# Optimization experiments

Measured on AMD Instinct MI355X. Metric: run time of the kernel, lower is better.

Reference implementation:

```python
import jax, jax.numpy as jnp
from jax import lax
import numpy as np

EPS = 1e-12      # F.normalize eps
TOP_N = 250      # top negatives selected
SMOOTH = 1e-5    # soft dice smooth


def _dilate10(m):
    # == 10 iterations of 3x3x3 binary max-pool dilation. m: [B,D,H,W] float.
    for _ in range(10):
        m = lax.reduce_window(m, 0.0, lax.max, (1, 3, 3, 3), (1, 1, 1, 1), 'SAME')
    return m


def _self_loss(feature, lab):
    # feature: [B,C,D,H,W], lab: [B,D,H,W] int
    feat = jnp.moveaxis(feature, 1, -1)                       # [B,D,H,W,C]
    pos = (lab == 1)
    posf = pos.astype(feat.dtype)
    cnt = posf.sum()
    std = (feat * posf[..., None]).sum((0, 1, 2, 3)) / jnp.maximum(cnt, 1.0)
    std = jnp.where(cnt > 0, std, 0.0)                        # [C]
    std_n = std / jnp.maximum(jnp.linalg.norm(std), EPS)
    feat_n = feat / jnp.maximum(jnp.linalg.norm(feat, axis=-1, keepdims=True), EPS)
    # cosine similarity of per-voxel normalized features vs normalized mean positive
    sim = jnp.einsum('bdhwc,c->bdhw', feat_n, std_n)

    # positive term: mean over positives of (1 - sim)
    pos_loss = jnp.where(cnt > 0, ((1.0 - sim) * posf).sum() / jnp.maximum(cnt, 1.0), 0.0)

    # easily-misclassified ring: dilate(pos,10) & ~pos; mean relu(sim)
    mis = (_dilate10(posf) > 0) & (~pos)
    misf = mis.astype(sim.dtype)
    mcnt = misf.sum()
    mis_loss = jnp.where(mcnt > 0, (jax.nn.relu(sim) * misf).sum() / jnp.maximum(mcnt, 1.0), 0.0)

    # hard negatives: top-250 sims among label==0, scatter to mask, dilate, & ~pos
    neg = (lab == 0)
    neg_sims = jnp.where(neg, sim, -jnp.inf).reshape(-1)
    top_vals, top_idx = lax.top_k(neg_sims, TOP_N)
    hsm = jnp.zeros(neg_sims.shape[0], sim.dtype).at[top_idx].set(
        jnp.where(jnp.isfinite(top_vals), 1.0, 0.0)).reshape(sim.shape)
    fin = (_dilate10(hsm) > 0) & (~pos)
    finf = fin.astype(sim.dtype)
    fcnt = finf.sum()
    neg_loss = jnp.where(fcnt > 0, (jax.nn.relu(sim) * finf).sum() / jnp.maximum(fcnt, 1.0), 0.0)

    return pos_loss + mis_loss + neg_loss


def _ce_dice(net_output, target):
    lab = target[:, 0]                                        # [B,D,H,W]
    logp = jax.nn.log_softmax(net_output, axis=1)
    ce = -jnp.mean(jnp.take_along_axis(logp, target, axis=1))
    probs = jnp.exp(logp)                                     # softmax_helper_dim1
    nc = net_output.shape[1]
    onehot = jax.nn.one_hot(lab, nc, axis=1, dtype=probs.dtype)  # [B,nc,D,H,W]
    axes = (0, 2, 3, 4)                                       # batch_dice=True
    tp = (probs * onehot).sum(axes)
    fp = (probs * (1.0 - onehot)).sum(axes)
    fn = ((1.0 - probs) * onehot).sum(axes)
    dc = (2.0 * tp + SMOOTH) / (2.0 * tp + fp + fn + SMOOTH + 1e-8)
    dice = -jnp.mean(dc[1:])                                  # do_bg=False
    return ce, dice


def reference(feature, net_output, target):
    ce, dice = _ce_dice(net_output, target)
    sl = _self_loss(feature, target[:, 0])
    return 1.0 * ce + 1.0 * dice + 5.0 * sl


def setup_inputs():
    key = jax.random.key(0)
    k1, k2, k3 = jax.random.split(key, 3)
    B, C, D, H, W = 2, 32, 64, 128, 128
    NC = 2
    feature = jax.random.normal(k1, (B, C, D, H, W), jnp.float32)
    net_output = jax.random.normal(k2, (B, NC, D, H, W), jnp.float32)
    target = jax.random.randint(k3, (B, 1, D, H, W), 0, 2).astype(jnp.int32)
    return {'feature': feature, 'net_output': net_output, 'target': target}
```

## Files before the change

### kernel.cpp

```cpp
#include <hip/hip_runtime.h>
#include <stdint.h>

typedef unsigned int u32;
typedef unsigned long long u64;
typedef float f4v __attribute__((ext_vector_type(4)));
typedef int i4v __attribute__((ext_vector_type(4)));

#define BB 2
#define CC 32
#define DD 64
#define HH 128
#define WW 128
#define SS (DD*HH*WW)
#define NN (BB*SS)
#define NQ (NN/4)
#define NWORDS (NN/64)
#define EPSF 1e-12f
#define TOPN 250u

struct Ctrl {
  u32 done4, tie, pad0, pad1;
};

struct Acc {
  double ce, tp, fp, fn;
  double stdsum[CC];
  double pos_num, mis_num, fin_num;
  u64 cnt, mcnt, fcnt;
};

__device__ __forceinline__ float waveRedF(float v){
#pragma unroll
  for (int o = 32; o; o >>= 1) v += __shfl_xor(v, o);
  return v;
}
__device__ __forceinline__ u32 waveRedU(u32 v){
#pragma unroll
  for (int o = 32; o; o >>= 1) v += __shfl_xor(v, o);
  return v;
}
__device__ __forceinline__ void red_d(double* dst, float v, volatile float* sh){
  int lane = threadIdx.x & 63, wid = threadIdx.x >> 6;
  v = waveRedF(v);
  if (lane == 0) sh[wid] = v;
  __syncthreads();
  if (threadIdx.x == 0){
    float t = 0.f;
    for (int i = 0; i < (int)(blockDim.x >> 6); i++) t += sh[i];
    atomicAdd(dst, (double)t);
  }
  __syncthreads();
}
__device__ __forceinline__ void red_u(u64* dst, u32 v, volatile u32* sh){
  int lane = threadIdx.x & 63, wid = threadIdx.x >> 6;
  v = waveRedU(v);
  if (lane == 0) sh[wid] = v;
  __syncthreads();
  if (threadIdx.x == 0){
    u32 t = 0;
    for (int i = 0; i < (int)(blockDim.x >> 6); i++) t += sh[i];
    atomicAdd(dst, (u64)t);
  }
  __syncthreads();
}

__device__ __forceinline__ u32 sortkey(float f){
  u32 u = __float_as_uint(f);
  return (u & 0x80000000u) ? ~u : (u | 0x80000000u);
}

__device__ __forceinline__ void select_top(const u32* __restrict__ hist, u32 nbins,
                                           u32 k, u32* shres, u32* binOut, u32* kremOut){
  __syncthreads();
  if (threadIdx.x < 64){
    int lane = threadIdx.x;
    u32 running = 0; bool found = false;
    for (u32 chunk = 0; chunk * 64 < nbins && !found; chunk++){
      int bin = (int)nbins - 1 - (int)(chunk * 64 + (u32)lane);
      u32 val = (bin >= 0) ? hist[bin] : 0u;
      u32 p = val;
#pragma unroll
      for (int o = 1; o < 64; o <<= 1){ u32 t = __shfl_up(p, o); if (lane >= o) p += t; }
      u32 tot = __shfl(p, 63);
      u32 incl = running + p, excl = incl - val;
      bool hit = (excl < k) && (incl >= k);
      u64 mb = __ballot(hit);
      if (mb){
        int hl = __ffsll((unsigned long long)mb) - 1;
        if (lane == hl){ shres[0] = (u32)bin; shres[1] = k - excl; }
        found = true;
      } else running += tot;
    }
    if (!found && lane == 0){ shres[0] = 0; shres[1] = k; }
  }
  __syncthreads();
  *binOut = shres[0]; *kremOut = shres[1];
}

__global__ __launch_bounds__(256) void k_pre(const int* __restrict__ tgt,
                                             u64* __restrict__ pbits,
                                             u32* __restrict__ cntArr,
                                             u32* __restrict__ zptr, u32 zwords){
  __shared__ u32 nibsh[256];
  __shared__ u32 shu[4];
  if (blockIdx.x == 0){
    for (u32 i = threadIdx.x; i < zwords; i += 256u) zptr[i] = 0;
  }
  u32 cnt = 0;
#pragma unroll 1
  for (u32 it = 0; it < 4; it++){
    u32 q = blockIdx.x * 1024u + it * 256u + threadIdx.x;
    i4v l4 = __builtin_nontemporal_load((const i4v*)(tgt + q * 4u));
    u32 nib = (l4.x ? 1u : 0u) | (l4.y ? 2u : 0u) | (l4.z ? 4u : 0u) | (l4.w ? 8u : 0u);
    cnt += __popc(nib);
    __syncthreads();
    nibsh[threadIdx.x] = nib;
    __syncthreads();
    if (threadIdx.x < 16){
      u64 o = 0;
#pragma unroll
      for (int j = 0; j < 16; j++)
        o |= (u64)(nibsh[threadIdx.x * 16 + j] & 0xFu) << (4 * j);
      pbits[blockIdx.x * 64u + it * 16u + threadIdx.x] = o;
    }
  }
  int lane = threadIdx.x & 63, wid = threadIdx.x >> 6;
  cnt = waveRedU(cnt);
  if (lane == 0) shu[wid] = cnt;
  __syncthreads();
  if (threadIdx.x == 0) cntArr[blockIdx.x] = shu[0] + shu[1] + shu[2] + shu[3];
}

__global__ __launch_bounds__(256) void k_ce_std(const float* __restrict__ feat,
                                                const float* __restrict__ net,
                                                const u64* __restrict__ pbits, Acc* acc){
  __shared__ float sh[16];
  if (blockIdx.x < 64u){
    u32 bid = blockIdx.x;
    float ce = 0.f, tp = 0.f, fp = 0.f, fnn = 0.f;
#pragma unroll 1
    for (u32 it = 0; it < 32; it++){
      u32 q = bid * 8192u + it * 256u + threadIdx.x;
      u32 nib = (u32)(pbits[q >> 4] >> ((q & 15u) << 2)) & 0xFu;
      u32 v = q * 4u;
      u32 b = v >> 20, s = v & (SS - 1);
      const float* nb = net + (size_t)(b * 2) * SS + s;
      f4v x0 = __builtin_nontemporal_load((const f4v*)(nb));
      f4v x1 = __builtin_nontemporal_load((const f4v*)(nb + SS));
      float xs0[4] = {x0.x, x0.y, x0.z, x0.w};
      float xs1[4] = {x1.x, x1.y, x1.z, x1.w};
#pragma unroll
      for (int j = 0; j < 4; j++){
        int lab = (nib >> j) & 1;
        float m = fmaxf(xs0[j], xs1[j]);
        float lse = m + logf(expf(xs0[j] - m) + expf(xs1[j] - m));
        ce += lse - (lab ? xs1[j] : xs0[j]);
        float p1 = expf(xs1[j] - lse);
        if (lab){ tp += p1; fnn += 1.0f - p1; } else fp += p1;
      }
    }
    int lane = threadIdx.x & 63, wid = threadIdx.x >> 6;
    ce = waveRedF(ce); tp = waveRedF(tp); fp = waveRedF(fp); fnn = waveRedF(fnn);
    if (lane == 0){ sh[wid] = ce; sh[4 + wid] = tp; sh[8 + wid] = fp; sh[12 + wid] = fnn; }
    __syncthreads();
    if (threadIdx.x == 0){
      atomicAdd(&acc->ce, (double)(sh[0] + sh[1] + sh[2] + sh[3]));
      atomicAdd(&acc->tp, (double)(sh[4] + sh[5] + sh[6] + sh[7]));
      atomicAdd(&acc->fp, (double)(sh[8] + sh[9] + sh[10] + sh[11]));
      atomicAdd(&acc->fn, (double)(sh[12] + sh[13] + sh[14] + sh[15]));
    }
  } else {
    u32 bx = blockIdx.x - 64u;
    u32 c = bx & 31u;
    u32 chunk = bx >> 5;
    u32 vbase = chunk * 65536u;
    u32 b = vbase >> 20;
    u32 s0 = vbase & (SS - 1);
    const float* fp_ = feat + (size_t)b * CC * SS + (size_t)c * SS + s0;
    const u64* pb = pbits + (vbase >> 6);
    float a = 0.f;
#pragma unroll 8
    for (u32 i = 0; i < 64; i++){
      u32 off = i * 1024u + threadIdx.x * 4u;
      float4 f = *(const float4*)(fp_ + off);
      u32 bits = (u32)(pb[off >> 6] >> (off & 63u)) & 0xFu;
      if (bits & 1u) a += f.x;
      if (bits & 2u) a += f.y;
      if (bits & 4u) a += f.z;
      if (bits & 8u) a += f.w;
    }
    int lane = threadIdx.x & 63, wid = threadIdx.x >> 6;
    a = waveRedF(a);
    if (lane == 0) sh[wid] = a;
    __syncthreads();
    if (threadIdx.x == 0)
      atomicAdd(&acc->stdsum[c], (double)(sh[0] + sh[1] + sh[2] + sh[3]));
  }
}

__global__ __launch_bounds__(256) void k_sim(const float* __restrict__ feat,
                                             const u64* __restrict__ pbits,
                                             const u32* __restrict__ cntArr,
                                             Acc* acc, float* __restrict__ sim,
                                             u32* __restrict__ h1){
  __shared__ float st[CC];
  __shared__ u32 lh[2048];
  __shared__ float shf[4];
  __shared__ u32 scnt;
  if (threadIdx.x < 64){
    u32 sc = 0;
#pragma unroll
    for (int i = 0; i < 8; i++) sc += cntArr[threadIdx.x * 8 + i];
    sc = waveRedU(sc);
    if (threadIdx.x == 0) scnt = sc;
  }
  __syncthreads();
  u32 cnt = scnt;
  if (blockIdx.x == 0 && threadIdx.x == 0) acc->cnt = (u64)cnt;
  {
    float sv = 0.f;
    if (threadIdx.x < CC && cnt) sv = (float)(acc->stdsum[threadIdx.x] / (double)cnt);
    if (threadIdx.x < 64){
      float t = waveRedF(sv * sv);
      float d = fmaxf(sqrtf(t), EPSF);
      if (threadIdx.x < CC) st[threadIdx.x] = sv / d;
    }
  }
  for (u32 i = threadIdx.x; i < 2048u; i += 256u) lh[i] = 0;
  __syncthreads();
  u32 vbase = (511u - blockIdx.x) * 4096u;
  u32 b = vbase >> 20;
  u32 s0 = vbase & (SS - 1);
  const float* fp = feat + (size_t)b * CC * SS + s0;
  float4 dt[4], n2[4];
#pragma unroll
  for (int g = 0; g < 4; g++){
    dt[g].x = dt[g].y = dt[g].z = dt[g].w = 0.f;
    n2[g].x = n2[g].y = n2[g].z = n2[g].w = 0.f;
  }
#pragma unroll 2
  for (u32 c = 0; c < CC; c++){
    float w = st[c];
    const float* fc = fp + (size_t)c * SS;
    float4 f[4];
#pragma unroll
    for (int g = 0; g < 4; g++)
      f[g] = *(const float4*)(fc + (u32)g * 1024u + threadIdx.x * 4u);
#pragma unroll
    for (int g = 0; g < 4; g++){
      dt[g].x += f[g].x * w; dt[g].y += f[g].y * w;
      dt[g].z += f[g].z * w; dt[g].w += f[g].w * w;
      n2[g].x += f[g].x * f[g].x; n2[g].y += f[g].y * f[g].y;
      n2[g].z += f[g].z * f[g].z; n2[g].w += f[g].w * f[g].w;
    }
  }
  float pn = 0.f;
#pragma unroll
  for (int g = 0; g < 4; g++){
    u32 off = (u32)g * 1024u + threadIdx.x * 4u;
    u32 v = vbase + off;
    float4 sm;
    sm.x = dt[g].x / fmaxf(sqrtf(n2[g].x), EPSF);
    sm.y = dt[g].y / fmaxf(sqrtf(n2[g].y), EPSF);
    sm.z = dt[g].z / fmaxf(sqrtf(n2[g].z), EPSF);
    sm.w = dt[g].w / fmaxf(sqrtf(n2[g].w), EPSF);
    *(float4*)(sim + v) = sm;
    u32 bits = (u32)(pbits[v >> 6] >> (v & 63u)) & 0xFu;
    float ss[4] = {sm.x, sm.y, sm.z, sm.w};
#pragma unroll
    for (int j = 0; j < 4; j++){
      if ((bits >> j) & 1u) pn += 1.f - ss[j];
      else atomicAdd(&lh[sortkey(ss[j]) >> 21], 1u);
    }
  }
  __syncthreads();
  for (u32 i = threadIdx.x; i < 2048u; i += 256u)
    if (lh[i]) atomicAdd(&h1[i], lh[i]);
  red_d(&acc->pos_num, pn, shf);
}

__device__ __forceinline__ void dilwh_slab(const u64* __restrict__ in, u64* __restrict__ out,
                                           u32 slab, u64* arr){
  u32 base = slab * 256u;
  int t = threadIdx.x;
  if (t < 128){
    u64 lo = in[base + 2 * t], hi = in[base + 2 * t + 1];
    u64 al = lo, ah = hi;
#pragma unroll
    for (int i = 0; i < 10; i++){ u64 c = al >> 63; ah = ah | (ah << 1) | c; al = al | (al << 1); }
    u64 bl = lo, bh = hi;
#pragma unroll
    for (int i = 0; i < 10; i++){ u64 c = bh << 63; bl = bl | (bl >> 1) | c; bh = bh | (bh >> 1); }
    arr[2 * t] = al | bl;
    arr[2 * t + 1] = ah | bh;
  }
  __syncthreads();
  int h = t >> 1, wj = t & 1;
  int h0 = h - 10 > 0 ? h - 10 : 0;
  int h1 = h + 10 < 127 ? h + 10 : 127;
  u64 o = 0;
  for (int hh = h0; hh <= h1; hh++) o |= arr[2 * hh + wj];
  out[base + (u32)t] = o;
  __syncthreads();
}

__global__ __launch_bounds__(256) void k_dilwh(const u64* __restrict__ in, u64* __restrict__ out){
  __shared__ u64 arr[256];
  dilwh_slab(in, out, blockIdx.x, arr);
}

__global__ __launch_bounds__(256) void k_histL2(const float* __restrict__ sim,
                                                const u64* __restrict__ pbits,
                                                const u32* __restrict__ h1,
                                                u32* __restrict__ h2,
                                                const u64* __restrict__ P,
                                                u64* __restrict__ T1P){
  __shared__ u64 arr[256];
  __shared__ u32 lh[2048];
  __shared__ u32 shres[2];
  if (blockIdx.x < 128u) dilwh_slab(P, T1P, blockIdx.x, arr);
  u32 p1, k1;
  select_top(h1, 2048, TOPN, shres, &p1, &k1);
  for (u32 i = threadIdx.x; i < 2048u; i += 256u) lh[i] = 0;
  __syncthreads();
  const u32 stride = 512u * 256u;
#pragma unroll 1
  for (u32 it = 0; it < 4; it++){
    u32 q = blockIdx.x * 256u + threadIdx.x + it * stride;
    u32 nib = (u32)(pbits[q >> 4] >> ((q & 15u) << 2)) & 0xFu;
    float4 s4 = *(const float4*)(sim + q * 4u);
    float ss[4] = {s4.x, s4.y, s4.z, s4.w};
#pragma unroll
    for (int j = 0; j < 4; j++){
      if (!((nib >> j) & 1u)){
        u32 key = sortkey(ss[j]);
        if ((key >> 21) == p1) atomicAdd(&lh[(key >> 10) & 2047u], 1u);
      }
    }
  }
  __syncthreads();
  for (u32 i = threadIdx.x; i < 2048u; i += 256u)
    if (lh[i]) atomicAdd(&h2[i], lh[i]);
}

__global__ __launch_bounds__(256) void k_mark(const float* __restrict__ sim,
                                              const u64* __restrict__ pbits,
                                              u64* __restrict__ hs,
                                              const u32* __restrict__ h1,
                                              const u32* __restrict__ h2,
                                              Ctrl* ctrl){
  __shared__ u32 shres[2];
  u32 p1, k1, b2, k2;
  select_top(h1, 2048, TOPN, shres, &p1, &k1);
  select_top(h2, 2048, k1, shres, &b2, &k2);
  u32 p12 = (p1 << 11) | b2;
  int lane = threadIdx.x & 63;
  const u32 stride = 1024u * 256u;
#pragma unroll 1
  for (u32 it = 0; it < 8; it++){
    u32 v = blockIdx.x * 256u + threadIdx.x + it * stride;
    u64 w = pbits[v >> 6];
    bool neg = !((w >> (v & 63u)) & 1ull);
    bool seed = false;
    if (neg){
      u32 pref = sortkey(sim[v]) >> 10;
      if (pref > p12) seed = true;
      else if (pref == p12){
        u32 old = atomicAdd(&ctrl->tie, 1u);
        if (old < k2) seed = true;
      }
    }
    u64 mb = __ballot(seed);
    if (lane == 0) hs[v >> 6] = mb;
  }
}

__global__ __launch_bounds__(256) void k_final(const float* __restrict__ sim,
                                               const u64* __restrict__ P,
                                               const u64* __restrict__ T1P,
                                               const u64* __restrict__ T1H,
                                               Acc* acc, Ctrl* ctrl, float* out){
  __shared__ float shf[4]; __shared__ u32 shu[4];
  __shared__ int amLast;
  u32 wi = blockIdx.x * 256u + threadIdx.x;
  u32 wj = wi & 1u;
  u32 row = wi >> 1;
  int h = (int)(row & 127u);
  int d = (int)((row >> 7) & 63u);
  u32 b = row >> 13;
  int d0 = d - 10 > 0 ? d - 10 : 0;
  int d1 = d + 10 < 63 ? d + 10 : 63;
  const u64* bp = T1P + ((size_t)(b << 13) + (u32)h) * 2 + wj;
  const u64* bh = T1H + ((size_t)(b << 13) + (u32)h) * 2 + wj;
  u64 dpw = 0, dhw = 0;
  for (int dd = d0; dd <= d1; dd++){
    dpw |= bp[(size_t)dd * 256];
    dhw |= bh[(size_t)dd * 256];
  }
  u64 pw = P[wi];
  u64 mis = dpw & ~pw;
  u64 fin = dhw & ~pw;
  float mn = 0.f, fnm = 0.f;
  u32 mc = (u32)__popcll(mis), fc = (u32)__popcll(fin);
  const float* sp = sim + (size_t)wi * 64u;
#pragma unroll 1
  for (int jj = 0; jj < 16; jj++){
    float4 s4 = *(const float4*)(sp + jj * 4);
    float ss[4] = {s4.x, s4.y, s4.z, s4.w};
#pragma unroll
    for (int j = 0; j < 4; j++){
      int bit = jj * 4 + j;
      float r = fmaxf(ss[j], 0.f);
      if ((mis >> bit) & 1ull) mn += r;
      if ((fin >> bit) & 1ull) fnm += r;
    }
  }
  red_d(&acc->mis_num, mn, shf);
  red_d(&acc->fin_num, fnm, shf);
  red_u(&acc->mcnt, mc, shu);
  red_u(&acc->fcnt, fc, shu);
  __threadfence();
  if (threadIdx.x == 0) amLast = (atomicAdd(&ctrl->done4, 1u) == gridDim.x - 1);
  __syncthreads();
  if (amLast && threadIdx.x == 0){
    double ce = acc->ce / (double)NN;
    double tp = acc->tp, fp = acc->fp, fn = acc->fn;
    double dc1 = (2.0 * tp + 1e-5) / (2.0 * tp + fp + fn + 1e-5 + 1e-8);
    u64 cnt = acc->cnt;
    double pos_loss = cnt ? (acc->pos_num / (double)cnt) : 0.0;
    u64 mcnt = atomicAdd(&acc->mcnt, 0ull);
    u64 fcnt = atomicAdd(&acc->fcnt, 0ull);
    double mis_loss = mcnt ? (atomicAdd(&acc->mis_num, 0.0) / (double)mcnt) : 0.0;
    double neg_loss = fcnt ? (atomicAdd(&acc->fin_num, 0.0) / (double)fcnt) : 0.0;
    out[0] = (float)(ce - dc1 + 5.0 * (pos_loss + mis_loss + neg_loss));
  }
}

extern "C" void kernel_launch(void* const* d_in, const int* in_sizes, int n_in,
                              void* d_out, int out_size, void* d_ws, size_t ws_size,
                              hipStream_t stream){
  (void)in_sizes; (void)n_in; (void)out_size; (void)ws_size;
  const float* feat = (const float*)d_in[0];
  const float* net  = (const float*)d_in[1];
  const int*   tgt  = (const int*)d_in[2];
  float* out = (float*)d_out;
  char* ws = (char*)d_ws;

  size_t off = 0;
  auto take = [&](size_t bytes) -> void* {
    void* p = (void*)(ws + off);
    off += (bytes + 255) & ~(size_t)255;
    return p;
  };
  float* sim = (float*)take((size_t)NN * 4);
  u64* P   = (u64*)take((size_t)NWORDS * 8);
  u64* T1P = (u64*)take((size_t)NWORDS * 8);
  u64* HS  = (u64*)take((size_t)NWORDS * 8);
  u64* T1H = (u64*)take((size_t)NWORDS * 8);
  u32* cntArr = (u32*)take(512 * 4);
  size_t zstart = off;
  u32* h1 = (u32*)take(2048 * 4);
  u32* h2 = (u32*)take(2048 * 4);
  Ctrl* ctrl = (Ctrl*)take(sizeof(Ctrl));
  Acc* acc = (Acc*)take(sizeof(Acc));
  u32 zwords = (u32)((off - zstart) >> 2);

  k_pre<<<512, 256, 0, stream>>>(tgt, P, cntArr, (u32*)(ws + zstart), zwords);
  k_ce_std<<<1088, 256, 0, stream>>>(feat, net, P, acc);
  k_sim<<<512, 256, 0, stream>>>(feat, P, cntArr, acc, sim, h1);
  k_histL2<<<512, 256, 0, stream>>>(sim, P, h1, h2, P, T1P);
  k_mark<<<1024, 256, 0, stream>>>(sim, P, HS, h1, h2, ctrl);
  k_dilwh<<<128, 256, 0, stream>>>(HS, T1H);
  k_final<<<128, 256, 0, stream>>>(sim, P, T1P, T1H, acc, ctrl, out);
}
```

Measured before the change: 487.0 us.

## Fuse hard-negative marking with WH dilation and widen grids for streaming kernels

Merges k_mark and k_dilwh into one kernel, k_markdil. It builds the per-slab seed bitmask in LDS and dilates it in place, which removes the HS global buffer and one launch. It also doubles the block count of k_ce_std and quadruples that of k_sim, giving each block less work and adding launch-bounds occupancy hints. The aim is more parallelism for these memory-bound feature passes. The risks are that the fused mark kernel now runs only 128 blocks, and that k_sim issues four times as many histogram flushes and atomics.

```diff
diff --git a/kernel.cpp b/kernel.cpp
--- a/kernel.cpp
+++ b/kernel.cpp
@@ -95,6 +95,55 @@
   }
   __syncthreads();
   *binOut = shres[0]; *kremOut = shres[1];
+}
+
+__device__ __forceinline__ void dilwh_lds(const u64* hsw, u64* __restrict__ out,
+                                          u32 slab, u64* arr){
+  int t = threadIdx.x;
+  if (t < 128){
+    u64 lo = hsw[2 * t], hi = hsw[2 * t + 1];
+    u64 al = lo, ah = hi;
+#pragma unroll
+    for (int i = 0; i < 10; i++){ u64 c = al >> 63; ah = ah | (ah << 1) | c; al = al | (al << 1); }
+    u64 bl = lo, bh = hi;
+#pragma unroll
+    for (int i = 0; i < 10; i++){ u64 c = bh << 63; bl = bl | (bl >> 1) | c; bh = bh | (bh >> 1); }
+    arr[2 * t] = al | bl;
+    arr[2 * t + 1] = ah | bh;
+  }
+  __syncthreads();
+  int h = t >> 1, wj = t & 1;
+  int h0 = h - 10 > 0 ? h - 10 : 0;
+  int h1 = h + 10 < 127 ? h + 10 : 127;
+  u64 o = 0;
+  for (int hh = h0; hh <= h1; hh++) o |= arr[2 * hh + wj];
+  out[slab * 256u + (u32)t] = o;
+  __syncthreads();
+}
+
+__device__ __forceinline__ void dilwh_slab(const u64* __restrict__ in, u64* __restrict__ out,
+                                           u32 slab, u64* arr){
+  u32 base = slab * 256u;
+  int t = threadIdx.x;
+  if (t < 128){
+    u64 lo = in[base + 2 * t], hi = in[base + 2 * t + 1];
+    u64 al = lo, ah = hi;
+#pragma unroll
+    for (int i = 0; i < 10; i++){ u64 c = al >> 63; ah = ah | (ah << 1) | c; al = al | (al << 1); }
+    u64 bl = lo, bh = hi;
+#pragma unroll
+    for (int i = 0; i < 10; i++){ u64 c = bh << 63; bl = bl | (bl >> 1) | c; bh = bh | (bh >> 1); }
+    arr[2 * t] = al | bl;
+    arr[2 * t + 1] = ah | bh;
+  }
+  __syncthreads();
+  int h = t >> 1, wj = t & 1;
+  int h0 = h - 10 > 0 ? h - 10 : 0;
+  int h1 = h + 10 < 127 ? h + 10 : 127;
+  u64 o = 0;
+  for (int hh = h0; hh <= h1; hh++) o |= arr[2 * hh + wj];
+  out[base + (u32)t] = o;
+  __syncthreads();
 }
 
 __global__ __launch_bounds__(256) void k_pre(const int* __restrict__ tgt,
@@ -131,16 +180,16 @@
   if (threadIdx.x == 0) cntArr[blockIdx.x] = shu[0] + shu[1] + shu[2] + shu[3];
 }
 
-__global__ __launch_bounds__(256) void k_ce_std(const float* __restrict__ feat,
-                                                const float* __restrict__ net,
-                                                const u64* __restrict__ pbits, Acc* acc){
+__global__ __launch_bounds__(256, 8) void k_ce_std(const float* __restrict__ feat,
+                                                   const float* __restrict__ net,
+                                                   const u64* __restrict__ pbits, Acc* acc){
   __shared__ float sh[16];
-  if (blockIdx.x < 64u){
+  if (blockIdx.x < 128u){
     u32 bid = blockIdx.x;
     float ce = 0.f, tp = 0.f, fp = 0.f, fnn = 0.f;
-#pragma unroll 1
-    for (u32 it = 0; it < 32; it++){
-      u32 q = bid * 8192u + it * 256u + threadIdx.x;
+#pragma unroll 2
+    for (u32 it = 0; it < 16; it++){
+      u32 q = bid * 4096u + it * 256u + threadIdx.x;
       u32 nib = (u32)(pbits[q >> 4] >> ((q & 15u) << 2)) & 0xFu;
       u32 v = q * 4u;
       u32 b = v >> 20, s = v & (SS - 1);
@@ -170,17 +219,17 @@
       atomicAdd(&acc->fn, (double)(sh[12] + sh[13] + sh[14] + sh[15]));
     }
   } else {
-    u32 bx = blockIdx.x - 64u;
+    u32 bx = blockIdx.x - 128u;
     u32 c = bx & 31u;
     u32 chunk = bx >> 5;
-    u32 vbase = chunk * 65536u;
+    u32 vbase = chunk * 32768u;
     u32 b = vbase >> 20;
     u32 s0 = vbase & (SS - 1);
     const float* fp_ = feat + (size_t)b * CC * SS + (size_t)c * SS + s0;
     const u64* pb = pbits + (vbase >> 6);
     float a = 0.f;
-#pragma unroll 8
-    for (u32 i = 0; i < 64; i++){
+#pragma unroll 4
+    for (u32 i = 0; i < 32; i++){
       u32 off = i * 1024u + threadIdx.x * 4u;
       float4 f = *(const float4*)(fp_ + off);
       u32 bits = (u32)(pb[off >> 6] >> (off & 63u)) & 0xFu;
@@ -198,11 +247,11 @@
   }
 }
 
-__global__ __launch_bounds__(256) void k_sim(const float* __restrict__ feat,
-                                             const u64* __restrict__ pbits,
-                                             const u32* __restrict__ cntArr,
-                                             Acc* acc, float* __restrict__ sim,
-                                             u32* __restrict__ h1){
+__global__ __launch_bounds__(256, 8) void k_sim(const float* __restrict__ feat,
+                                                const u64* __restrict__ pbits,
+                                                const u32* __restrict__ cntArr,
+                                                Acc* acc, float* __restrict__ sim,
+                                                u32* __restrict__ h1){
   __shared__ float st[CC];
   __shared__ u32 lh[2048];
   __shared__ float shf[4];
@@ -228,42 +277,26 @@
   }
   for (u32 i = threadIdx.x; i < 2048u; i += 256u) lh[i] = 0;
   __syncthreads();
-  u32 vbase = (511u - blockIdx.x) * 4096u;
+  u32 vbase = blockIdx.x * 1024u;
   u32 b = vbase >> 20;
   u32 s0 = vbase & (SS - 1);
-  const float* fp = feat + (size_t)b * CC * SS + s0;
-  float4 dt[4], n2[4];
-#pragma unroll
-  for (int g = 0; g < 4; g++){
-    dt[g].x = dt[g].y = dt[g].z = dt[g].w = 0.f;
-    n2[g].x = n2[g].y = n2[g].z = n2[g].w = 0.f;
-  }
-#pragma unroll 2
+  const float* fp = feat + (size_t)b * CC * SS + s0 + threadIdx.x * 4u;
+  float4 dt = {0.f, 0.f, 0.f, 0.f}, n2 = {0.f, 0.f, 0.f, 0.f};
+#pragma unroll 4
   for (u32 c = 0; c < CC; c++){
     float w = st[c];
-    const float* fc = fp + (size_t)c * SS;
-    float4 f[4];
-#pragma unroll
-    for (int g = 0; g < 4; g++)
-      f[g] = *(const float4*)(fc + (u32)g * 1024u + threadIdx.x * 4u);
-#pragma unroll
-    for (int g = 0; g < 4; g++){
-      dt[g].x += f[g].x * w; dt[g].y += f[g].y * w;
-      dt[g].z += f[g].z * w; dt[g].w += f[g].w * w;
-      n2[g].x += f[g].x * f[g].x; n2[g].y += f[g].y * f[g].y;
-      n2[g].z += f[g].z * f[g].z; n2[g].w += f[g].w * f[g].w;
-    }
+    float4 f = *(const float4*)(fp + (size_t)c * SS);
+    dt.x += f.x * w; dt.y += f.y * w; dt.z += f.z * w; dt.w += f.w * w;
+    n2.x += f.x * f.x; n2.y += f.y * f.y; n2.z += f.z * f.z; n2.w += f.w * f.w;
   }
   float pn = 0.f;
-#pragma unroll
-  for (int g = 0; g < 4; g++){
-    u32 off = (u32)g * 1024u + threadIdx.x * 4u;
-    u32 v = vbase + off;
+  {
+    u32 v = vbase + threadIdx.x * 4u;
     float4 sm;
-    sm.x = dt[g].x / fmaxf(sqrtf(n2[g].x), EPSF);
-    sm.y = dt[g].y / fmaxf(sqrtf(n2[g].y), EPSF);
-    sm.z = dt[g].z / fmaxf(sqrtf(n2[g].z), EPSF);
-    sm.w = dt[g].w / fmaxf(sqrtf(n2[g].w), EPSF);
+    sm.x = dt.x / fmaxf(sqrtf(n2.x), EPSF);
+    sm.y = dt.y / fmaxf(sqrtf(n2.y), EPSF);
+    sm.z = dt.z / fmaxf(sqrtf(n2.z), EPSF);
+    sm.w = dt.w / fmaxf(sqrtf(n2.w), EPSF);
     *(float4*)(sim + v) = sm;
     u32 bits = (u32)(pbits[v >> 6] >> (v & 63u)) & 0xFu;
     float ss[4] = {sm.x, sm.y, sm.z, sm.w};
@@ -277,36 +310,6 @@
   for (u32 i = threadIdx.x; i < 2048u; i += 256u)
     if (lh[i]) atomicAdd(&h1[i], lh[i]);
   red_d(&acc->pos_num, pn, shf);
-}
-
-__device__ __forceinline__ void dilwh_slab(const u64* __restrict__ in, u64* __restrict__ out,
-                                           u32 slab, u64* arr){
-  u32 base = slab * 256u;
-  int t = threadIdx.x;
-  if (t < 128){
-    u64 lo = in[base + 2 * t], hi = in[base + 2 * t + 1];
-    u64 al = lo, ah = hi;
-#pragma unroll
-    for (int i = 0; i < 10; i++){ u64 c = al >> 63; ah = ah | (ah << 1) | c; al = al | (al << 1); }
-    u64 bl = lo, bh = hi;
-#pragma unroll
-    for (int i = 0; i < 10; i++){ u64 c = bh << 63; bl = bl | (bl >> 1) | c; bh = bh | (bh >> 1); }
-    arr[2 * t] = al | bl;
-    arr[2 * t + 1] = ah | bh;
-  }
-  __syncthreads();
-  int h = t >> 1, wj = t & 1;
-  int h0 = h - 10 > 0 ? h - 10 : 0;
-  int h1 = h + 10 < 127 ? h + 10 : 127;
-  u64 o = 0;
-  for (int hh = h0; hh <= h1; hh++) o |= arr[2 * hh + wj];
-  out[base + (u32)t] = o;
-  __syncthreads();
-}
-
-__global__ __launch_bounds__(256) void k_dilwh(const u64* __restrict__ in, u64* __restrict__ out){
-  __shared__ u64 arr[256];
-  dilwh_slab(in, out, blockIdx.x, arr);
 }
 
 __global__ __launch_bounds__(256) void k_histL2(const float* __restrict__ sim,
@@ -343,24 +346,27 @@
     if (lh[i]) atomicAdd(&h2[i], lh[i]);
 }
 
-__global__ __launch_bounds__(256) void k_mark(const float* __restrict__ sim,
-                                              const u64* __restrict__ pbits,
-                                              u64* __restrict__ hs,
-                                              const u32* __restrict__ h1,
-                                              const u32* __restrict__ h2,
-                                              Ctrl* ctrl){
+__global__ __launch_bounds__(256) void k_markdil(const float* __restrict__ sim,
+                                                 const u64* __restrict__ pbits,
+                                                 const u32* __restrict__ h1,
+                                                 const u32* __restrict__ h2,
+                                                 u64* __restrict__ T1H,
+                                                 Ctrl* ctrl){
   __shared__ u32 shres[2];
+  __shared__ u64 hsw[256];
+  __shared__ u64 arr[256];
   u32 p1, k1, b2, k2;
   select_top(h1, 2048, TOPN, shres, &p1, &k1);
   select_top(h2, 2048, k1, shres, &b2, &k2);
   u32 p12 = (p1 << 11) | b2;
-  int lane = threadIdx.x & 63;
-  const u32 stride = 1024u * 256u;
-#pragma unroll 1
-  for (u32 it = 0; it < 8; it++){
-    u32 v = blockIdx.x * 256u + threadIdx.x + it * stride;
-    u64 w = pbits[v >> 6];
-    bool neg = !((w >> (v & 63u)) & 1ull);
+  int lane = threadIdx.x & 63, wid = threadIdx.x >> 6;
+  u32 slab = blockIdx.x;
+#pragma unroll 4
+  for (u32 i = 0; i < 64; i++){
+    u32 w = (u32)wid * 64u + i;
+    u32 v = slab * 16384u + w * 64u + (u32)lane;
+    u64 pw = pbits[v >> 6];
+    bool neg = !((pw >> (v & 63u)) & 1ull);
     bool seed = false;
     if (neg){
       u32 pref = sortkey(sim[v]) >> 10;
@@ -371,8 +377,10 @@
       }
     }
     u64 mb = __ballot(seed);
-    if (lane == 0) hs[v >> 6] = mb;
-  }
+    if (lane == 0) hsw[w] = mb;
+  }
+  __syncthreads();
+  dilwh_lds(hsw, T1H, slab, arr);
 }
 
 __global__ __launch_bounds__(256) void k_final(const float* __restrict__ sim,
@@ -455,7 +463,6 @@
   float* sim = (float*)take((size_t)NN * 4);
   u64* P   = (u64*)take((size_t)NWORDS * 8);
   u64* T1P = (u64*)take((size_t)NWORDS * 8);
-  u64* HS  = (u64*)take((size_t)NWORDS * 8);
   u64* T1H = (u64*)take((size_t)NWORDS * 8);
   u32* cntArr = (u32*)take(512 * 4);
   size_t zstart = off;
@@ -466,10 +473,9 @@
   u32 zwords = (u32)((off - zstart) >> 2);
 
   k_pre<<<512, 256, 0, stream>>>(tgt, P, cntArr, (u32*)(ws + zstart), zwords);
-  k_ce_std<<<1088, 256, 0, stream>>>(feat, net, P, acc);
-  k_sim<<<512, 256, 0, stream>>>(feat, P, cntArr, acc, sim, h1);
+  k_ce_std<<<2176, 256, 0, stream>>>(feat, net, P, acc);
+  k_sim<<<2048, 256, 0, stream>>>(feat, P, cntArr, acc, sim, h1);
   k_histL2<<<512, 256, 0, stream>>>(sim, P, h1, h2, P, T1P);
-  k_mark<<<1024, 256, 0, stream>>>(sim, P, HS, h1, h2, ctrl);
-  k_dilwh<<<128, 256, 0, stream>>>(HS, T1H);
+  k_markdil<<<128, 256, 0, stream>>>(sim, P, h1, h2, T1H, ctrl);
   k_final<<<128, 256, 0, stream>>>(sim, P, T1P, T1H, acc, ctrl, out);
 }
```

Result: slower. 525.5 us (+7.9%).
